# Performance work log

Hardware: AMD Instinct MI355X
Metric: run time of the kernel (lower is better)

The kernel has to match this reference:

```python
import jax, jax.numpy as jnp
import numpy as np

EMBED_DIM = 1024
NUM_HEADS = 16
WINDOW = 128  # one-sided window length w; total span 2w+1


def setup_inputs() -> dict:
    key = jax.random.key(0)
    ks = jax.random.split(key, 9)
    D = EMBED_DIM
    x = jax.random.normal(ks[0], (2, 8192, D), dtype=jnp.float32)
    s = 0.02
    Wq = jax.random.normal(ks[1], (D, D), dtype=jnp.float32) * s
    bq = jax.random.normal(ks[2], (D,), dtype=jnp.float32) * s
    Wk = jax.random.normal(ks[3], (D, D), dtype=jnp.float32) * s
    bk = jax.random.normal(ks[4], (D,), dtype=jnp.float32) * s
    Wv = jax.random.normal(ks[5], (D, D), dtype=jnp.float32) * s
    bv = jax.random.normal(ks[6], (D,), dtype=jnp.float32) * s
    Wo = jax.random.normal(ks[7], (D, D), dtype=jnp.float32) * s
    bo = jax.random.normal(ks[8], (D,), dtype=jnp.float32) * s
    return {"x": x, "Wq": Wq, "bq": bq, "Wk": Wk, "bk": bk,
            "Wv": Wv, "bv": bv, "Wo": Wo, "bo": bo}


def _sliding_window_attention(x, Wq, bq, Wk, bk, Wv, bv, Wo, bo):
    B, S, D = x.shape
    H, w = NUM_HEADS, WINDOW
    hd = D // H
    bs = w            # block size = window_length; 3 blocks cover [i-w, i+w]
    nb = S // bs

    def proj(W, b):
        y = x @ W.T + b                              # torch Linear: x @ W.T + b
        return y.reshape(B, S, H, hd).transpose(0, 2, 1, 3)  # [B,H,S,hd]

    q = proj(Wq, bq)
    k = proj(Wk, bk)
    v = proj(Wv, bv)

    qb = q.reshape(B, H, nb, bs, hd)
    # pad K/V with one zero block on each side, then build 3-block contexts
    pad = ((0, 0), (0, 0), (bs, bs), (0, 0))
    kp = jnp.pad(k, pad).reshape(B, H, nb + 2, bs, hd)
    vp = jnp.pad(v, pad).reshape(B, H, nb + 2, bs, hd)
    k_ctx = jnp.concatenate([kp[:, :, :-2], kp[:, :, 1:-1], kp[:, :, 2:]], axis=3)  # [B,H,nb,3bs,hd]
    v_ctx = jnp.concatenate([vp[:, :, :-2], vp[:, :, 1:-1], vp[:, :, 2:]], axis=3)

    scale = 1.0 / np.sqrt(hd).astype(np.float32)
    scores = jnp.einsum('bhnqd,bhnkd->bhnqk', qb, k_ctx) * scale  # [B,H,nb,bs,3bs]

    # band mask: |k_pos - q_pos| <= w, and k_pos in [0, S)
    q_off = jnp.arange(bs)
    k_off = jnp.arange(3 * bs)
    rel = k_off[None, :] - bs - q_off[:, None]                # [bs,3bs]
    win_ok = jnp.abs(rel) <= w
    k_pos = (jnp.arange(nb)[:, None, None] - 1) * bs + k_off[None, None, :]
    valid = (k_pos >= 0) & (k_pos < S)                        # [nb,1,3bs]
    mask = win_ok[None] & valid                               # [nb,bs,3bs]

    scores = jnp.where(mask[None, None], scores, jnp.float32(-jnp.inf))
    weights = jax.nn.softmax(scores, axis=-1)

    out = jnp.einsum('bhnqk,bhnkd->bhnqd', weights, v_ctx)    # [B,H,nb,bs,hd]
    out = out.reshape(B, H, S, hd).transpose(0, 2, 1, 3).reshape(B, S, D)
    return out @ Wo.T + bo


def reference(x, Wq, bq, Wk, bk, Wv, bv, Wo, bo):
    return _sliding_window_attention(x, Wq, bq, Wk, bk, Wv, bv, Wo, bo)
```

## Files before the change

### kernel.cpp

```cpp
#include <hip/hip_runtime.h>

typedef __attribute__((ext_vector_type(4))) float f32x4;
typedef __attribute__((ext_vector_type(8))) short s16x8;

#define MFMA16(a, b, c) __builtin_amdgcn_mfma_f32_16x16x32_bf16((a), (b), (c), 0, 0, 0)

__device__ __forceinline__ unsigned short f2bf_bits(float f) {
  unsigned int u = __float_as_uint(f);
  unsigned int r = (u + 0x7fffu + ((u >> 16) & 1u)) >> 16;
  return (unsigned short)r;
}

__device__ __forceinline__ void gl_lds16(const void* g, void* l) {
  __builtin_amdgcn_global_load_lds((const __attribute__((address_space(1))) void*)g,
                                   (__attribute__((address_space(3))) void*)l, 16, 0, 0);
}

__device__ __forceinline__ unsigned lds_off(const void* p) {
  return (unsigned)(unsigned long long)p;
}

template <int IMM>
__device__ __forceinline__ s16x8 dsr(unsigned base) {
  s16x8 r;
  asm volatile("ds_read_b128 %0, %1 offset:%2" : "=v"(r) : "v"(base), "n"(IMM));
  return r;
}

__global__ __launch_bounds__(256) void f2bf_kernel(const float* __restrict__ in,
                                                   unsigned short* __restrict__ out, int n4) {
  int idx = blockIdx.x * 256 + threadIdx.x;
  int stride = gridDim.x * 256;
  for (int i = idx; i < n4; i += stride) {
    float4 v = ((const float4*)in)[i];
    ushort4 o;
    o.x = f2bf_bits(v.x); o.y = f2bf_bits(v.y);
    o.z = f2bf_bits(v.z); o.w = f2bf_bits(v.w);
    ((ushort4*)out)[i] = o;
  }
}

__global__ __launch_bounds__(256) void f2bf_w4(const float* __restrict__ w0,
                                               const float* __restrict__ w1,
                                               const float* __restrict__ w2,
                                               const float* __restrict__ w3,
                                               unsigned short* __restrict__ o0,
                                               unsigned short* __restrict__ o1,
                                               unsigned short* __restrict__ o2,
                                               unsigned short* __restrict__ o3) {
  const int s = blockIdx.y;
  const float* in = (s == 0) ? w0 : (s == 1) ? w1 : (s == 2) ? w2 : w3;
  unsigned short* out = (s == 0) ? o0 : (s == 1) ? o1 : (s == 2) ? o2 : o3;
  int i = blockIdx.x * 256 + threadIdx.x;
  float4 v = ((const float4*)in)[i];
  ushort4 o;
  o.x = f2bf_bits(v.x); o.y = f2bf_bits(v.y);
  o.z = f2bf_bits(v.z); o.w = f2bf_bits(v.w);
  ((ushort4*)out)[i] = o;
}


#define S_BAR __builtin_amdgcn_s_barrier()
#define WAIT_LGKM0 asm volatile("s_waitcnt lgkmcnt(0)")
#define SCHED_FENCE __builtin_amdgcn_sched_barrier(0)
#define PRIO1 __builtin_amdgcn_s_setprio(1)
#define PRIO0 __builtin_amdgcn_s_setprio(0)
#define VM_W2 asm volatile("s_waitcnt vmcnt(2)")
#define VM_W0 asm volatile("s_waitcnt vmcnt(0)")
#define VM_NONE

#define STAGE2(gsrc, ldsdst)                                    \
  gl_lds16((gsrc), (ldsdst) + (size_t)tid * 8);                 \
  gl_lds16((gsrc) + 65536, (ldsdst) + (size_t)tid * 8 + 4096);

#define RD_A03(ax0, ax1)                                        \
  afA[0][0] = dsr<0>(ax0);      afA[0][1] = dsr<0>(ax1);        \
  afA[1][0] = dsr<2048>(ax0);   afA[1][1] = dsr<2048>(ax1);     \
  afA[2][0] = dsr<4096>(ax0);   afA[2][1] = dsr<4096>(ax1);     \
  afA[3][0] = dsr<6144>(ax0);   afA[3][1] = dsr<6144>(ax1);
#define RD_A47(ax0, ax1)                                        \
  afB[0][0] = dsr<8192>(ax0);   afB[0][1] = dsr<8192>(ax1);     \
  afB[1][0] = dsr<10240>(ax0);  afB[1][1] = dsr<10240>(ax1);    \
  afB[2][0] = dsr<12288>(ax0);  afB[2][1] = dsr<12288>(ax1);    \
  afB[3][0] = dsr<14336>(ax0);  afB[3][1] = dsr<14336>(ax1);
#define RD_B01(bx0, bx1)                                        \
  bf[0][0] = dsr<0>(bx0);       bf[0][1] = dsr<0>(bx1);         \
  bf[1][0] = dsr<2048>(bx0);    bf[1][1] = dsr<2048>(bx1);
#define RD_B23(bx0, bx1)                                        \
  bf[2][0] = dsr<4096>(bx0);    bf[2][1] = dsr<4096>(bx1);      \
  bf[3][0] = dsr<6144>(bx0);    bf[3][1] = dsr<6144>(bx1);

#define MM_BLOCK(AF, MB, NB)                                                          \
  _Pragma("unroll") for (int m_ = 0; m_ < 4; ++m_)                                    \
    _Pragma("unroll") for (int n_ = 0; n_ < 2; ++n_) {                                \
      acc[(MB) + m_][(NB) + n_] =                                                     \
          MFMA16(AF[m_][0], bf[(NB) + n_][0], acc[(MB) + m_][(NB) + n_]);             \
      acc[(MB) + m_][(NB) + n_] =                                                     \
          MFMA16(AF[m_][1], bf[(NB) + n_][1], acc[(MB) + m_][(NB) + n_]);             \
    }

#define TILE_M201(T_, AC0, AC1, BC0, BC1, ALO_, BLC_, STA_, STB_, VMW_)        \
                                      \
  RD_A03(AC0, AC1);                                                             \
  RD_B01(BC0, BC1);                                                             \
  if (STA_) { STAGE2(gA + ((T_) + 1) * 64, (ALO_)); }                           \
  S_BAR; WAIT_LGKM0; SCHED_FENCE;                                               \
  PRIO1; MM_BLOCK(afA, 0, 0); PRIO0;                                            \
  S_BAR;                                                                        \
                                              \
  RD_B23(BC0, BC1);                                                             \
  if (STA_) { STAGE2(gA + 131072 + ((T_) + 1) * 64, (ALO_) + 8192); }           \
  S_BAR; WAIT_LGKM0; SCHED_FENCE;                                               \
  PRIO1; MM_BLOCK(afA, 0, 2); PRIO0;                                            \
  S_BAR;                                                                        \
       \
  RD_A47(AC0, AC1);                                                             \
  if (STB_) { STAGE2(gB + ((T_) + 2) * 64, (BLC_)); }                           \
  S_BAR; WAIT_LGKM0; SCHED_FENCE;                                               \
  PRIO1; MM_BLOCK(afB, 4, 0); PRIO0;                                            \
  VMW_;                                                                         \
  S_BAR;                                                                        \
    \
  if (STB_) { STAGE2(gB + 131072 + ((T_) + 2) * 64, (BLC_) + 8192); }           \
  SCHED_FENCE;                                                                  \
  PRIO1; MM_BLOCK(afB, 4, 2); PRIO0;

#define GEMM256_CORE(Ab_, Bb_)                                                        \
  f32x4 acc[8][4];                                                                    \
  _Pragma("unroll") for (int mi = 0; mi < 8; ++mi)                                    \
      _Pragma("unroll") for (int ni = 0; ni < 4; ++ni)                                \
          acc[mi][ni] = (f32x4){0.f, 0.f, 0.f, 0.f};                                  \
  s16x8 afA[4][2], afB[4][2], bf[4][2];                                               \
  {                                                                                   \
    const int r_ = tid >> 3;                                                          \
    const int c_ = (tid & 7) ^ (r_ & 7);                                              \
    const unsigned short* gA = (Ab_) + (size_t)r_ * 1024 + c_ * 8;                    \
    const unsigned short* gB = (Bb_) + (size_t)r_ * 1024 + c_ * 8;                    \
    const unsigned x0 = (unsigned)((quad ^ (l15 & 7)) * 16);                          \
    const unsigned x1 = (unsigned)(((4 + quad) ^ (l15 & 7)) * 16);                    \
    const unsigned aW = (unsigned)(l15 * 128);                                        \
    const unsigned bW = (unsigned)(bro * 128 + l15 * 128);                            \
    const unsigned a0x0 = lds_off(&Al[0][wm][0]) + aW + x0;                           \
    const unsigned a0x1 = lds_off(&Al[0][wm][0]) + aW + x1;                           \
    const unsigned a1x0 = lds_off(&Al[1][wm][0]) + aW + x0;                           \
    const unsigned a1x1 = lds_off(&Al[1][wm][0]) + aW + x1;                           \
    const unsigned b0x0 = lds_off(&Bl[0][wn >> 1][0]) + bW + x0;                      \
    const unsigned b0x1 = lds_off(&Bl[0][wn >> 1][0]) + bW + x1;                      \
    const unsigned b1x0 = lds_off(&Bl[1][wn >> 1][0]) + bW + x0;                      \
    const unsigned b1x1 = lds_off(&Bl[1][wn >> 1][0]) + bW + x1;                      \
                   \
    STAGE2(gA, (&Al[0][0][0]));                                                       \
    STAGE2(gA + 131072, (&Al[0][0][0]) + 8192);                                       \
    STAGE2(gB, (&Bl[0][0][0]));                                                       \
    STAGE2(gB + 131072, (&Bl[0][0][0]) + 8192);                                       \
    STAGE2(gB + 64, (&Bl[1][0][0]));                                                  \
    STAGE2(gB + 131072 + 64, (&Bl[1][0][0]) + 8192);                                  \
    SCHED_FENCE;                                                                      \
    asm volatile("s_waitcnt vmcnt(4)");             \
    S_BAR; SCHED_FENCE;                                                               \
    _Pragma("unroll 1") for (int Tp = 0; Tp < 7; ++Tp) {                              \
      const int T0 = Tp * 2;                                                          \
      TILE_M201(T0, a0x0, a0x1, b0x0, b0x1, (&Al[1][0][0]), (&Bl[0][0][0]),           \
                1, 1, VM_W2);                                                         \
      TILE_M201(T0 + 1, a1x0, a1x1, b1x0, b1x1, (&Al[0][0][0]), (&Bl[1][0][0]),       \
                1, 1, VM_W2);                                                         \
    }                                                                                 \
                                 \
    TILE_M201(14, a0x0, a0x1, b0x0, b0x1, (&Al[1][0][0]), (&Bl[0][0][0]),             \
              1, 0, VM_W0);                                                           \
                                              \
    TILE_M201(15, a1x0, a1x1, b1x0, b1x1, (&Al[0][0][0]), (&Bl[1][0][0]),             \
              0, 0, VM_NONE);                                                         \
  }

__global__ __launch_bounds__(512, 2) void gemm_qkv(const unsigned short* __restrict__ A,
                                                   const unsigned short* __restrict__ Wq,
                                                   const unsigned short* __restrict__ Wk,
                                                   const unsigned short* __restrict__ Wv,
                                                   const float* __restrict__ bq,
                                                   const float* __restrict__ bk,
                                                   const float* __restrict__ bv,
                                                   unsigned short* __restrict__ Qo,
                                                   unsigned short* __restrict__ Ko,
                                                   unsigned short* __restrict__ Vt) {
  __shared__ unsigned short Al[2][2][8192];
  __shared__ unsigned short Bl[2][2][8192];
  const int tid = threadIdx.x;
  const int lane = tid & 63, wave = tid >> 6;
  const int l15 = lane & 15, quad = lane >> 4;
  const int wm = wave >> 2, wn = wave & 3;
  const int bro = (wn & 1) * 64;
  const int bx = blockIdx.x;
  const int sel = blockIdx.y >> 2, byl = blockIdx.y & 3;

  const unsigned short* W = (sel == 0) ? Wq : (sel == 1) ? Wk : Wv;
  const float* bias = (sel == 0) ? bq : (sel == 1) ? bk : bv;
  const unsigned short* Ab = A + (size_t)bx * 256 * 1024;
  const unsigned short* Bb = W + (size_t)byl * 256 * 1024;

  GEMM256_CORE(Ab, Bb)

#pragma unroll
  for (int nf = 0; nf < 4; ++nf) {
    const int cn = byl * 256 + wn * 64 + nf * 16 + l15;
    const float bj = bias[cn];
#pragma unroll
    for (int mf = 0; mf < 8; ++mf) {
      const int r0 = bx * 256 + wm * 128 + mf * 16 + quad * 4;
#pragma unroll
      for (int r = 0; r < 4; ++r) {
        const int row = r0 + r;
        const float v = acc[mf][nf][r] + bj;
        if (sel == 0) {
          Qo[(size_t)row * 1024 + cn] = f2bf_bits(v);
        } else if (sel == 1) {
          Ko[(size_t)row * 1024 + cn] = f2bf_bits(v);
        } else {
          Vt[((size_t)(row >> 13) * 1024 + cn) * 8192 + (row & 8191)] = f2bf_bits(v);
        }
      }
    }
  }
}

__global__ __launch_bounds__(512, 2) void gemm_out(const unsigned short* __restrict__ A,
                                                   const unsigned short* __restrict__ B,
                                                   const float* __restrict__ bias,
                                                   float* __restrict__ Cf) {
  __shared__ unsigned short Al[2][2][8192];
  __shared__ unsigned short Bl[2][2][8192];
  const int tid = threadIdx.x;
  const int lane = tid & 63, wave = tid >> 6;
  const int l15 = lane & 15, quad = lane >> 4;
  const int wm = wave >> 2, wn = wave & 3;
  const int bro = (wn & 1) * 64;
  const int bx = blockIdx.x;

  const unsigned short* Ab = A + (size_t)bx * 256 * 1024;
  const unsigned short* Bb = B + (size_t)blockIdx.y * 256 * 1024;

  GEMM256_CORE(Ab, Bb)

#pragma unroll
  for (int nf = 0; nf < 4; ++nf) {
    const int cn = blockIdx.y * 256 + wn * 64 + nf * 16 + l15;
    const float bj = bias[cn];
#pragma unroll
    for (int mf = 0; mf < 8; ++mf) {
      const int r0 = bx * 256 + wm * 128 + mf * 16 + quad * 4;
#pragma unroll
      for (int r = 0; r < 4; ++r) Cf[(size_t)(r0 + r) * 1024 + cn] = acc[mf][nf][r] + bj;
    }
  }
}

__global__ __launch_bounds__(256, 3) void attn_kernel(const unsigned short* __restrict__ Q,
                                                      const unsigned short* __restrict__ Km,
                                                      const unsigned short* __restrict__ Vt,
                                                      unsigned short* __restrict__ O) {
  const int n = blockIdx.x;
  const int bh = blockIdx.y;
  const int b = bh >> 4, h = bh & 15;
  const int tid = threadIdx.x, lane = tid & 63, wave = tid >> 6;
  const int l15 = lane & 15, quad = lane >> 4;

  __shared__ unsigned short Kl[384 * 64];
  __shared__ unsigned short Ps[4][16 * 40];

  const int base_row = n * 128 - 128;

  for (int i = 0; i < 12; ++i) {
    const int c = i * 256 + tid;
    const int row = c >> 3;
    const int qc = (c & 7) ^ (row & 7);
    int gr = base_row + row;
    gr = min(max(gr, 0), 8191);
    gl_lds16(Km + (size_t)(b * 8192 + gr) * 1024 + h * 64 + qc * 8, &Kl[c * 8]);
  }
  __syncthreads();

  const unsigned short* Vbase = Vt + (size_t)bh * 64 * 8192;
  unsigned short* strip = &Ps[wave][0];

  for (int mt = 0; mt < 2; ++mt) {
    const int qt = wave * 2 + mt;
    const int q0 = n * 128 + qt * 16;
    const int qp = q0 + l15;

    const unsigned short* qptr = Q + (size_t)(b * 8192 + qp) * 1024 + h * 64 + quad * 8;
    const s16x8 bq0 = *(const s16x8*)qptr;
    const s16x8 bq1 = *(const s16x8*)(qptr + 32);

    f32x4 o[4];
#pragma unroll
    for (int dt = 0; dt < 4; ++dt) o[dt] = (f32x4){0.f, 0.f, 0.f, 0.f};
    float lsum = 0.f;

    const int krel0 = qt * 16;

#pragma unroll 1
    for (int p = 0; p < 9; ++p) {
      f32x4 st[2];
#pragma unroll
      for (int tt = 0; tt < 2; ++tt) {
        int rel = krel0 + p * 32 + tt * 16 + l15;
        int rr = min(rel, 383);
        const int ro = rr * 8;
        const int sw = rr & 7;
        const s16x8 ka0 = *(const s16x8*)&Kl[(ro + (quad ^ sw)) * 8];
        const s16x8 ka1 = *(const s16x8*)&Kl[(ro + ((4 + quad) ^ sw)) * 8];
        f32x4 a = (f32x4){0.f, 0.f, 0.f, 0.f};
        a = MFMA16(ka0, bq0, a);
        a = MFMA16(ka1, bq1, a);
        st[tt] = a;
      }
      ushort4 w0, w1;
#pragma unroll
      for (int tt = 0; tt < 2; ++tt) {
        unsigned short* wp = tt ? (unsigned short*)&w1 : (unsigned short*)&w0;
#pragma unroll
        for (int r = 0; r < 4; ++r) {
          const int kp = base_row + krel0 + p * 32 + tt * 16 + quad * 4 + r;
          const int dd = kp - qp;
          const bool ok = (kp >= 0) && (kp < 8192) && (dd >= -128) && (dd <= 128);
          const float pv = ok ? __expf(st[tt][r] * 0.125f) : 0.f;
          lsum += pv;
          wp[r] = f2bf_bits(pv);
        }
      }
      *(ushort4*)&strip[l15 * 40 + quad * 4] = w0;
      *(ushort4*)&strip[l15 * 40 + 16 + quad * 4] = w1;
      const s16x8 pf = *(const s16x8*)&strip[l15 * 40 + quad * 8];
      int kc = base_row + krel0 + p * 32 + quad * 8;
      kc = min(max(kc, 0), 8184);
#pragma unroll
      for (int dt = 0; dt < 4; ++dt) {
        const s16x8 va = *(const s16x8*)(Vbase + (size_t)(dt * 16 + l15) * 8192 + kc);
        o[dt] = MFMA16(va, pf, o[dt]);
      }
    }

    lsum += __shfl_xor(lsum, 16, 64);
    lsum += __shfl_xor(lsum, 32, 64);
    const float rinv = 1.f / lsum;
    unsigned short* obase = O + (size_t)(b * 8192 + qp) * 1024 + h * 64;
#pragma unroll
    for (int dt = 0; dt < 4; ++dt) {
      ushort4 w;
      unsigned short* wp = (unsigned short*)&w;
#pragma unroll
      for (int r = 0; r < 4; ++r) wp[r] = f2bf_bits(o[dt][r] * rinv);
      *(ushort4*)(obase + dt * 16 + quad * 4) = w;
    }
  }
}

extern "C" void kernel_launch(void* const* d_in, const int* in_sizes, int n_in, void* d_out,
                              int out_size, void* d_ws, size_t ws_size, hipStream_t stream) {
  const float* x = (const float*)d_in[0];
  const float* Wq = (const float*)d_in[1];
  const float* bq = (const float*)d_in[2];
  const float* Wk = (const float*)d_in[3];
  const float* bk = (const float*)d_in[4];
  const float* Wv = (const float*)d_in[5];
  const float* bv = (const float*)d_in[6];
  const float* Wo = (const float*)d_in[7];
  const float* bo = (const float*)d_in[8];
  float* out = (float*)d_out;

  const int M = 16384, D = 1024;

  unsigned short* xb = (unsigned short*)d_ws;
  unsigned short* qb = xb + (size_t)M * D;
  unsigned short* kb = qb + (size_t)M * D;
  unsigned short* vt = kb + (size_t)M * D;
  unsigned short* ab = vt + (size_t)M * D;
  unsigned short* wqb = ab + (size_t)M * D;
  unsigned short* wkb = wqb + (size_t)D * D;
  unsigned short* wvb = wkb + (size_t)D * D;
  unsigned short* wob = wvb + (size_t)D * D;

  f2bf_kernel<<<16384, 256, 0, stream>>>(x, xb, M * D / 4);
  f2bf_w4<<<dim3(1024, 4), 256, 0, stream>>>(Wq, Wk, Wv, Wo, wqb, wkb, wvb, wob);

  gemm_qkv<<<dim3(M / 256, 12), 512, 0, stream>>>(xb, wqb, wkb, wvb, bq, bk, bv, qb, kb, vt);

  attn_kernel<<<dim3(64, 32), 256, 0, stream>>>(qb, kb, vt, ab);

  gemm_out<<<dim3(M / 256, D / 256), 512, 0, stream>>>(ab, wob, bo, out);
}
```

Before: 400.1 us.

## Prefetch A and B two tiles ahead with uniform double-buffer staging

Restructures the GEMM main loop's global-to-LDS pipeline. Both the A and B tiles are now prefetched two k-steps ahead into the same buffer just consumed, instead of A one step ahead and B two steps ahead. Staging moves to the second half of each tile, and the wait allows eight loads in flight. The aim is to give more latency slack for global loads and balance the issue slots. The risk is overwriting LDS that other waves still read, since it depends on barrier placement, and more outstanding loads.

```diff
diff --git a/kernel.cpp b/kernel.cpp
--- a/kernel.cpp
+++ b/kernel.cpp
@@ -65,7 +65,7 @@
 #define SCHED_FENCE __builtin_amdgcn_sched_barrier(0)
 #define PRIO1 __builtin_amdgcn_s_setprio(1)
 #define PRIO0 __builtin_amdgcn_s_setprio(0)
-#define VM_W2 asm volatile("s_waitcnt vmcnt(2)")
+#define VM_W8 asm volatile("s_waitcnt vmcnt(8)")
 #define VM_W0 asm volatile("s_waitcnt vmcnt(0)")
 #define VM_NONE
 
@@ -99,31 +99,36 @@
           MFMA16(AF[m_][1], bf[(NB) + n_][1], acc[(MB) + m_][(NB) + n_]);             \
     }
 
-#define TILE_M201(T_, AC0, AC1, BC0, BC1, ALO_, BLC_, STA_, STB_, VMW_)        \
-                                      \
+#define TILE_V4(T_, AC0, AC1, BC0, BC1, ALD_, BLD_, STG_, VMW_)                \
+                                                     \
   RD_A03(AC0, AC1);                                                             \
   RD_B01(BC0, BC1);                                                             \
-  if (STA_) { STAGE2(gA + ((T_) + 1) * 64, (ALO_)); }                           \
   S_BAR; WAIT_LGKM0; SCHED_FENCE;                                               \
   PRIO1; MM_BLOCK(afA, 0, 0); PRIO0;                                            \
   S_BAR;                                                                        \
-                                              \
+                                                             \
   RD_B23(BC0, BC1);                                                             \
-  if (STA_) { STAGE2(gA + 131072 + ((T_) + 1) * 64, (ALO_) + 8192); }           \
   S_BAR; WAIT_LGKM0; SCHED_FENCE;                                               \
   PRIO1; MM_BLOCK(afA, 0, 2); PRIO0;                                            \
   S_BAR;                                                                        \
-       \
+          \
   RD_A47(AC0, AC1);                                                             \
-  if (STB_) { STAGE2(gB + ((T_) + 2) * 64, (BLC_)); }                           \
+  if (STG_) {                                                                   \
+    STAGE2(gB + ((T_) + 2) * 64, (BLD_));                                       \
+    STAGE2(gB + 131072 + ((T_) + 2) * 64, (BLD_) + 8192);                       \
+  }                                                                             \
   S_BAR; WAIT_LGKM0; SCHED_FENCE;                                               \
   PRIO1; MM_BLOCK(afB, 4, 0); PRIO0;                                            \
+  S_BAR;                                                                        \
+       \
+  if (STG_) {                                                                   \
+    STAGE2(gA + ((T_) + 2) * 64, (ALD_));                                       \
+    STAGE2(gA + 131072 + ((T_) + 2) * 64, (ALD_) + 8192);                       \
+  }                                                                             \
+  SCHED_FENCE;                                                                  \
+  PRIO1; MM_BLOCK(afB, 4, 2); PRIO0;                                            \
   VMW_;                                                                         \
-  S_BAR;                                                                        \
-    \
-  if (STB_) { STAGE2(gB + 131072 + ((T_) + 2) * 64, (BLC_) + 8192); }           \
-  SCHED_FENCE;                                                                  \
-  PRIO1; MM_BLOCK(afB, 4, 2); PRIO0;
+  S_BAR;
 
 #define GEMM256_CORE(Ab_, Bb_)                                                        \
   f32x4 acc[8][4];                                                                    \
@@ -148,29 +153,31 @@
     const unsigned b0x1 = lds_off(&Bl[0][wn >> 1][0]) + bW + x1;                      \
     const unsigned b1x0 = lds_off(&Bl[1][wn >> 1][0]) + bW + x0;                      \
     const unsigned b1x1 = lds_off(&Bl[1][wn >> 1][0]) + bW + x1;                      \
-                   \
+         \
     STAGE2(gA, (&Al[0][0][0]));                                                       \
     STAGE2(gA + 131072, (&Al[0][0][0]) + 8192);                                       \
     STAGE2(gB, (&Bl[0][0][0]));                                                       \
     STAGE2(gB + 131072, (&Bl[0][0][0]) + 8192);                                       \
+    STAGE2(gA + 64, (&Al[1][0][0]));                                                  \
+    STAGE2(gA + 131072 + 64, (&Al[1][0][0]) + 8192);                                  \
     STAGE2(gB + 64, (&Bl[1][0][0]));                                                  \
     STAGE2(gB + 131072 + 64, (&Bl[1][0][0]) + 8192);                                  \
     SCHED_FENCE;                                                                      \
-    asm volatile("s_waitcnt vmcnt(4)");             \
+    asm volatile("s_waitcnt vmcnt(8)");        \
     S_BAR; SCHED_FENCE;                                                               \
     _Pragma("unroll 1") for (int Tp = 0; Tp < 7; ++Tp) {                              \
       const int T0 = Tp * 2;                                                          \
-      TILE_M201(T0, a0x0, a0x1, b0x0, b0x1, (&Al[1][0][0]), (&Bl[0][0][0]),           \
-                1, 1, VM_W2);                                                         \
-      TILE_M201(T0 + 1, a1x0, a1x1, b1x0, b1x1, (&Al[0][0][0]), (&Bl[1][0][0]),       \
-                1, 1, VM_W2);                                                         \
+      TILE_V4(T0, a0x0, a0x1, b0x0, b0x1, (&Al[0][0][0]), (&Bl[0][0][0]),             \
+              1, VM_W8);                                                              \
+      TILE_V4(T0 + 1, a1x0, a1x1, b1x0, b1x1, (&Al[1][0][0]), (&Bl[1][0][0]),         \
+              1, VM_W8);                                                              \
     }                                                                                 \
-                                 \
-    TILE_M201(14, a0x0, a0x1, b0x0, b0x1, (&Al[1][0][0]), (&Bl[0][0][0]),             \
-              1, 0, VM_W0);                                                           \
-                                              \
-    TILE_M201(15, a1x0, a1x1, b1x0, b1x1, (&Al[0][0][0]), (&Bl[1][0][0]),             \
-              0, 0, VM_NONE);                                                         \
+                       \
+    TILE_V4(14, a0x0, a0x1, b0x0, b0x1, (&Al[0][0][0]), (&Bl[0][0][0]),               \
+            0, VM_W0);                                                                \
+                                                \
+    TILE_V4(15, a1x0, a1x1, b1x0, b1x1, (&Al[1][0][0]), (&Bl[1][0][0]),               \
+            0, VM_NONE);                                                              \
   }
 
 __global__ __launch_bounds__(512, 2) void gemm_qkv(const unsigned short* __restrict__ A,
```

New measurement: 410.3 us. 2.6% more time.
